# Performance work log

Measured on AMD Instinct MI355X. Metric: run time of the kernel, lower is better.

The kernel has to match this reference:

```python
import jax, jax.numpy as jnp
import numpy as np

N = 4194304
C = 10

def setup_inputs() -> dict:
    key = jax.random.key(0)
    k1, k2 = jax.random.split(key)
    predicted = jax.random.normal(k1, (N, C), dtype=jnp.float32)
    target = jax.random.uniform(k2, (N, C), dtype=jnp.float32)
    return {"predicted": predicted, "target": target}

def reference(predicted, target):
    # Equivalent to: for y in range(C): cum += target[:, y] * cross_entropy(pred, y)
    # i.e. mean over points of -sum_y target[:, y] * log_softmax(pred)[:, y]
    logp = jax.nn.log_softmax(predicted, axis=-1)  # [N, C]
    cum_losses = -jnp.sum(target * logp, axis=-1)  # [N]
    return jnp.mean(cum_losses)
```

## Files before the change

### kernel.cpp

```cpp
#include <hip/hip_runtime.h>
#include <hip/hip_bf16.h>


#define N_ROWS 4194304
#define C_DIM 10
#define BLOCK 256
#define ROWS_PER_BLOCK 512
#define WORDS_PER_BLOCK (ROWS_PER_BLOCK * C_DIM)
#define F4_PER_THREAD 5
#define LDS_PAD 513

typedef float v4f __attribute__((ext_vector_type(4)));

__global__ void kl_loss_kernel(
    const float* __restrict__ pred,
    const float* __restrict__ tgt,
    float* __restrict__ out)
{
    __shared__ float sp[C_DIM][LDS_PAD];
    __shared__ float slse[ROWS_PER_BLOCK];
    __shared__ float sred[BLOCK / 64];

    const int tid = threadIdx.x;
    const size_t blk_f4 = (size_t)blockIdx.x * (WORDS_PER_BLOCK / 4);

    const v4f* p4 = reinterpret_cast<const v4f*>(pred);
    const v4f* t4 = reinterpret_cast<const v4f*>(tgt);

    v4f pv[F4_PER_THREAD], tv[F4_PER_THREAD];
#pragma unroll
    for (int i = 0; i < F4_PER_THREAD; ++i)
        pv[i] = __builtin_nontemporal_load(&p4[blk_f4 + i * BLOCK + tid]);
#pragma unroll
    for (int i = 0; i < F4_PER_THREAD; ++i)
        tv[i] = __builtin_nontemporal_load(&t4[blk_f4 + i * BLOCK + tid]);

#pragma unroll
    for (int i = 0; i < F4_PER_THREAD; ++i) {
        int w = (i * BLOCK + tid) * 4;
        int r = w / C_DIM;
        int y = w - r * C_DIM;
#pragma unroll
        for (int c = 0; c < 4; ++c) {
            sp[y][r] = pv[i][c];
            ++y;
            if (y == C_DIM) { y = 0; ++r; }
        }
    }
    __syncthreads();

#pragma unroll
    for (int half = 0; half < 2; ++half) {
        int r = tid + half * BLOCK;
        float x[C_DIM];
#pragma unroll
        for (int y = 0; y < C_DIM; ++y) x[y] = sp[y][r];
        float m = x[0];
#pragma unroll
        for (int y = 1; y < C_DIM; ++y) m = fmaxf(m, x[y]);
        float s = 0.0f;
#pragma unroll
        for (int y = 0; y < C_DIM; ++y) s += __expf(x[y] - m);
        slse[r] = m + __logf(s);
    }
    __syncthreads();

    float acc = 0.0f;
#pragma unroll
    for (int i = 0; i < F4_PER_THREAD; ++i) {
        int w = (i * BLOCK + tid) * 4;
        int r = w / C_DIM;
        int y = w - r * C_DIM;
#pragma unroll
        for (int c = 0; c < 4; ++c) {
            acc = fmaf(tv[i][c], slse[r] - pv[i][c], acc);
            ++y;
            if (y == C_DIM) { y = 0; ++r; }
        }
    }

#pragma unroll
    for (int off = 32; off > 0; off >>= 1)
        acc += __shfl_down(acc, off, 64);

    const int lane = tid & 63;
    const int wid  = tid >> 6;
    if (lane == 0) sred[wid] = acc;
    __syncthreads();

    if (tid == 0) {
        float b = sred[0] + sred[1] + sred[2] + sred[3];
        atomicAdd(out, b * (1.0f / (float)N_ROWS));
    }
}

extern "C" void kernel_launch(void* const* d_in, const int* in_sizes, int n_in,
                              void* d_out, int out_size, void* d_ws, size_t ws_size,
                              hipStream_t stream)
{
    const float* pred = (const float*)d_in[0];
    const float* tgt  = (const float*)d_in[1];
    float* out = (float*)d_out;

    hipMemsetAsync(out, 0, sizeof(float), stream);

    const int blocks = N_ROWS / ROWS_PER_BLOCK;
    kl_loss_kernel<<<blocks, BLOCK, 0, stream>>>(pred, tgt, out);
}
```

Baseline: 367.0 us.

## Split loss into dot term and target-sum times LSE, two-pass reduction

Rewrites the per-element loss sum(t*(lse-p)) as sum(t)*lse - dot(t,p). The dot product is computed in registers, and the target values are transposed through LDS so each thread can sum the targets of its own rows. This removes the slse shared array and its indexed reads, but adds a second LDS transpose pass and an extra barrier. It also replaces the per-block atomicAdd and the memset with per-block partials in the workspace and a single-block reduce kernel, which adds a second launch but makes the result deterministic.

Result: faster. 302.0 us (-17.7%).

```diff
diff --git a/kernel.cpp b/kernel.cpp
--- a/kernel.cpp
+++ b/kernel.cpp
@@ -9,16 +9,17 @@
 #define WORDS_PER_BLOCK (ROWS_PER_BLOCK * C_DIM)
 #define F4_PER_THREAD 5
 #define LDS_PAD 513
+#define NBLOCKS (N_ROWS / ROWS_PER_BLOCK)
+#define RBLOCK 1024
 
 typedef float v4f __attribute__((ext_vector_type(4)));
 
 __global__ void kl_loss_kernel(
     const float* __restrict__ pred,
     const float* __restrict__ tgt,
-    float* __restrict__ out)
+    float* __restrict__ partial)
 {
     __shared__ float sp[C_DIM][LDS_PAD];
-    __shared__ float slse[ROWS_PER_BLOCK];
     __shared__ float sred[BLOCK / 64];
 
     const int tid = threadIdx.x;
@@ -35,6 +36,13 @@
     for (int i = 0; i < F4_PER_THREAD; ++i)
         tv[i] = __builtin_nontemporal_load(&t4[blk_f4 + i * BLOCK + tid]);
 
+    float dot = 0.0f;
+#pragma unroll
+    for (int i = 0; i < F4_PER_THREAD; ++i)
+#pragma unroll
+        for (int c = 0; c < 4; ++c)
+            dot = fmaf(tv[i][c], pv[i][c], dot);
+
 #pragma unroll
     for (int i = 0; i < F4_PER_THREAD; ++i) {
         int w = (i * BLOCK + tid) * 4;
@@ -49,9 +57,10 @@
     }
     __syncthreads();
 
+    float lse[2];
 #pragma unroll
     for (int half = 0; half < 2; ++half) {
-        int r = tid + half * BLOCK;
+        const int r = tid + half * BLOCK;
         float x[C_DIM];
 #pragma unroll
         for (int y = 0; y < C_DIM; ++y) x[y] = sp[y][r];
@@ -61,11 +70,10 @@
         float s = 0.0f;
 #pragma unroll
         for (int y = 0; y < C_DIM; ++y) s += __expf(x[y] - m);
-        slse[r] = m + __logf(s);
+        lse[half] = m + __logf(s);
     }
     __syncthreads();
 
-    float acc = 0.0f;
 #pragma unroll
     for (int i = 0; i < F4_PER_THREAD; ++i) {
         int w = (i * BLOCK + tid) * 4;
@@ -73,10 +81,21 @@
         int y = w - r * C_DIM;
 #pragma unroll
         for (int c = 0; c < 4; ++c) {
-            acc = fmaf(tv[i][c], slse[r] - pv[i][c], acc);
+            sp[y][r] = tv[i][c];
             ++y;
             if (y == C_DIM) { y = 0; ++r; }
         }
+    }
+    __syncthreads();
+
+    float acc = -dot;
+#pragma unroll
+    for (int half = 0; half < 2; ++half) {
+        const int r = tid + half * BLOCK;
+        float st = 0.0f;
+#pragma unroll
+        for (int y = 0; y < C_DIM; ++y) st += sp[y][r];
+        acc = fmaf(st, lse[half], acc);
     }
 
 #pragma unroll
@@ -88,9 +107,36 @@
     if (lane == 0) sred[wid] = acc;
     __syncthreads();
 
+    if (tid == 0)
+        partial[blockIdx.x] = sred[0] + sred[1] + sred[2] + sred[3];
+}
+
+__global__ __launch_bounds__(RBLOCK) void kl_reduce_kernel(
+    const float* __restrict__ partial,
+    float* __restrict__ out)
+{
+    __shared__ float sred[RBLOCK / 64];
+    const int tid = threadIdx.x;
+
+    float acc = 0.0f;
+#pragma unroll
+    for (int i = 0; i < NBLOCKS / RBLOCK; ++i)
+        acc += partial[i * RBLOCK + tid];
+
+#pragma unroll
+    for (int off = 32; off > 0; off >>= 1)
+        acc += __shfl_down(acc, off, 64);
+
+    const int lane = tid & 63;
+    const int wid  = tid >> 6;
+    if (lane == 0) sred[wid] = acc;
+    __syncthreads();
+
     if (tid == 0) {
-        float b = sred[0] + sred[1] + sred[2] + sred[3];
-        atomicAdd(out, b * (1.0f / (float)N_ROWS));
+        float b = 0.0f;
+#pragma unroll
+        for (int i = 0; i < RBLOCK / 64; ++i) b += sred[i];
+        out[0] = b * (1.0f / (float)N_ROWS);
     }
 }
 
@@ -101,9 +147,8 @@
     const float* pred = (const float*)d_in[0];
     const float* tgt  = (const float*)d_in[1];
     float* out = (float*)d_out;
+    float* partialbuf = (float*)d_ws;
 
-    hipMemsetAsync(out, 0, sizeof(float), stream);
-
-    const int blocks = N_ROWS / ROWS_PER_BLOCK;
-    kl_loss_kernel<<<blocks, BLOCK, 0, stream>>>(pred, tgt, out);
+    kl_loss_kernel<<<NBLOCKS, BLOCK, 0, stream>>>(pred, tgt, partialbuf);
+    kl_reduce_kernel<<<1, RBLOCK, 0, stream>>>(partialbuf, out);
 }
```
